# Performance work log

Hardware: AMD Instinct MI355X
Metric: run time of the kernel (lower is better)

Reference implementation:

```python
import jax, jax.numpy as jnp
import numpy as np

B, K, S, L, D, A = 16, 128, 64, 2, 256, 500  # batch, beam, stack, layers, hidden, max_actions


def setup_inputs() -> dict:
    key = jax.random.key(0)
    k = jax.random.split(key, 8)
    return {
        "gen_ll": jax.random.normal(k[0], (B, K), jnp.float32),
        "trees": jax.random.normal(k[1], (B, K, S, D), jnp.float32),
        "hiddens": jax.random.normal(k[2], (B, K, S + 1, L, D), jnp.float32),
        "cells": jax.random.normal(k[3], (B, K, S + 1, L, D), jnp.float32),
        "actions": jax.random.randint(k[4], (B, K, A), 0, 100, dtype=jnp.int64)
        if jax.config.jax_enable_x64 else jax.random.randint(k[4], (B, K, A), 0, 100),
        "actions_pos": jax.random.randint(k[5], (B, K), 0, A - 1),
        "pointer": jax.random.randint(k[6], (B, K), 0, S),
        "beam_widths": jax.random.randint(k[7], (B,), 1, K + 1),  # >= 1 active beam per batch
    }


def _gather_beam(x, sort_idx):
    # gather along beam dim (axis=1) with broadcast over trailing dims
    idx = sort_idx.reshape(sort_idx.shape + (1,) * (x.ndim - 2))
    return jnp.take_along_axis(x, idx, axis=1)


def reference(gen_ll, trees, hiddens, cells, actions, actions_pos, pointer, beam_widths):
    # BeamItems.shrink(): mask beams outside active width, sort by score desc,
    # then reorder every parallel tensor (stack + action path) by sort_idx.
    order = jnp.arange(K)
    active = order[None, :] < beam_widths[:, None]                    # [B, K] active_idx_mask
    gen_ll_m = jnp.where(active, gen_ll, -jnp.inf)
    sort_idx = jnp.argsort(-gen_ll_m, axis=1)                          # descending sort
    gen_ll_s = jnp.take_along_axis(gen_ll_m, sort_idx, axis=1)

    trees_s = _gather_beam(trees, sort_idx)                            # stack.sort_by
    hiddens_s = _gather_beam(hiddens, sort_idx)
    cells_s = _gather_beam(cells, sort_idx)
    actions_s = _gather_beam(actions, sort_idx)                        # action_path.sort_by
    actions_pos_s = jnp.take_along_axis(actions_pos, sort_idx, axis=1)
    pointer_s = jnp.take_along_axis(pointer, sort_idx, axis=1)         # stack_state.sort_by

    new_beam_widths = jnp.minimum(beam_widths, K)
    # BeamItems.marginal_probs(): logsumexp over active beams (inactive already -inf)
    marginal = jax.nn.logsumexp(gen_ll_s, axis=1)                      # [B]
    # ActionPath.prev_actions(): gather at actions_pos
    prev_actions = jnp.take_along_axis(actions_s, actions_pos_s[:, :, None], axis=2)[:, :, 0]

    return (gen_ll_s, trees_s, hiddens_s, cells_s, marginal,
            actions_s, actions_pos_s, pointer_s, prev_actions, new_beam_widths)
```

## Files before the change

kernel.cpp:

```cpp
#include <hip/hip_runtime.h>
#include <math.h>

#define B 16
#define K 128
#define S 64
#define L 2
#define D 256
#define A 500

#define ROW4_TREES 4096
#define ROW4_HID   8320
#define HALF4_HID  4160

#define NEG_BIG (-1.0e30f)

typedef float f32x4 __attribute__((ext_vector_type(4)));
typedef int   i32x4 __attribute__((ext_vector_type(4)));

#define OFF_GENLL 0
#define OFF_TREES 2048
#define OFF_HID   33556480
#define OFF_CELLS 101713920
#define OFF_MARG  169871360
#define OFF_ACT   169871376
#define OFF_APOS  170895376
#define OFF_PTR   170897424
#define OFF_PREV  170899472
#define OFF_NBW   170901520

#define NU_TREES 2048
#define NU_HC    8192
#define NU_BIG   (NU_TREES + NU_HC)
#define NB_ACT   (B * K)
#define GRID     (NU_BIG + NB_ACT + B)

template<int N4>
__device__ __forceinline__ void copy_unit(const f32x4* __restrict__ s,
                                          f32x4* __restrict__ d, int tid)
{
    constexpr int FULL = N4 / 256;
    constexpr int REM  = N4 % 256;
    for (int g = 0; g < FULL; g += 8) {
        f32x4 v[8];
#pragma unroll
        for (int i = 0; i < 8; ++i)
            v[i] = __builtin_nontemporal_load(&s[(g + i) * 256 + tid]);
#pragma unroll
        for (int i = 0; i < 8; ++i)
            __builtin_nontemporal_store(v[i], &d[(g + i) * 256 + tid]);
    }
    if (REM && tid < REM) {
        f32x4 v = __builtin_nontemporal_load(&s[FULL * 256 + tid]);
        __builtin_nontemporal_store(v, &d[FULL * 256 + tid]);
    }
}

__global__ void __launch_bounds__(256, 8)
k_fused(const float* __restrict__ gen_ll,
        const f32x4* __restrict__ trees,
        const f32x4* __restrict__ hiddens,
        const f32x4* __restrict__ cells,
        const int* __restrict__ actions,
        const int* __restrict__ actions_pos,
        const int* __restrict__ pointer,
        const int* __restrict__ beam_widths,
        float* __restrict__ out)
{
    __shared__ float key[K];
    __shared__ int   sidx[K];
    __shared__ float red[4];

    const int tid = threadIdx.x;
    const int bid = blockIdx.x;

    int type, b = 0, k = 0, r = 0;
    int which = 0, u2 = 0;
    if (bid < NU_BIG) {
        type = 2;
        if (bid < NU_TREES) {
            which = -1;
            r = bid; b = r >> 7; k = r & 127;
        } else {
            const int u = bid - NU_TREES;
            which = u >> 12;
            u2 = u & 4095;
            const int row = u2 >> 1;
            b = row >> 7; k = row & 127;
        }
    } else if (bid < NU_BIG + NB_ACT) {
        type = 1; r = bid - NU_BIG; b = r >> 7; k = r & 127;
    } else {
        type = 0; b = bid - (NU_BIG + NB_ACT);
    }

    const int w = beam_widths[b];
    if (tid < K) key[tid] = (tid < w) ? gen_ll[b * K + tid] : NEG_BIG;
    __syncthreads();
    if (tid < K) {
        const float my = key[tid];
        int rank = 0;
#pragma unroll 16
        for (int i = 0; i < K; ++i) {
            const float ki = key[i];
            rank += (ki > my) || (ki == my && i < tid);
        }
        sidx[rank] = tid;
    }
    __syncthreads();

    if (type == 2) {
        const int j = sidx[k];
        if (which < 0) {
            copy_unit<ROW4_TREES>(trees + (size_t)(b * K + j) * ROW4_TREES,
                                  (f32x4*)(out + OFF_TREES) + (size_t)r * ROW4_TREES,
                                  tid);
        } else {
            const int half = u2 & 1;
            const f32x4* src = (which ? cells : hiddens)
                             + ((size_t)(b * K + j) * 2 + half) * HALF4_HID;
            f32x4* dst = (f32x4*)(out + (which ? OFF_CELLS : OFF_HID))
                       + (size_t)u2 * HALF4_HID;
            copy_unit<HALF4_HID>(src, dst, tid);
        }
    } else if (type == 1) {
        const int j = sidx[k];
        const i32x4* s = (const i32x4*)actions + (size_t)(b * K + j) * 125;
        f32x4* d = (f32x4*)(out + OFF_ACT) + (size_t)r * 125;
        if (tid < 125) {
            const i32x4 v = __builtin_nontemporal_load(&s[tid]);
            f32x4 f;
            f.x = (float)v.x; f.y = (float)v.y; f.z = (float)v.z; f.w = (float)v.w;
            __builtin_nontemporal_store(f, &d[tid]);
        }
    } else {
        if (tid < K) {
            const int j = sidx[tid];
            out[OFF_GENLL + b * K + tid] = key[j];
            const int ap = actions_pos[b * K + j];
            out[OFF_APOS + b * K + tid] = (float)ap;
            out[OFF_PTR  + b * K + tid] = (float)pointer[b * K + j];
            out[OFF_PREV + b * K + tid] = (float)actions[(size_t)(b * K + j) * A + ap];
        }
        const float v = (tid < K) ? key[tid] : NEG_BIG;
        if (tid < 128) {
            float m = v;
#pragma unroll
            for (int mask = 32; mask >= 1; mask >>= 1)
                m = fmaxf(m, __shfl_xor(m, mask, 64));
            if ((tid & 63) == 0) red[tid >> 6] = m;
        }
        __syncthreads();
        const float m = fmaxf(red[0], red[1]);
        if (tid < 128) {
            float e = expf(v - m);
#pragma unroll
            for (int mask = 32; mask >= 1; mask >>= 1)
                e += __shfl_xor(e, mask, 64);
            if ((tid & 63) == 0) red[2 + (tid >> 6)] = e;
        }
        __syncthreads();
        if (tid == 0) {
            out[OFF_MARG + b] = m + logf(red[2] + red[3]);
            out[OFF_NBW + b] = (float)(w < K ? w : K);
        }
    }
}

extern "C" void kernel_launch(void* const* d_in, const int* in_sizes, int n_in,
                              void* d_out, int out_size, void* d_ws, size_t ws_size,
                              hipStream_t stream)
{
    const float* gen_ll      = (const float*)d_in[0];
    const float* trees       = (const float*)d_in[1];
    const float* hiddens     = (const float*)d_in[2];
    const float* cells       = (const float*)d_in[3];
    const int*   actions     = (const int*)d_in[4];
    const int*   actions_pos = (const int*)d_in[5];
    const int*   pointer     = (const int*)d_in[6];
    const int*   beam_widths = (const int*)d_in[7];
    float* out = (float*)d_out;

    k_fused<<<GRID, 256, 0, stream>>>(gen_ll, (const f32x4*)trees,
                                      (const f32x4*)hiddens, (const f32x4*)cells,
                                      actions, actions_pos, pointer, beam_widths, out);
}
```

Before: 259.8 us.

## Use fixed 2048-block grid with multiple copy units per block

Replaces one-block-per-unit launch (about 12k blocks) with 2048 persistent-style blocks that each copy five row units plus one actions row. Every block now ranks all 16 batches' keys in shared memory instead of one batch. The aim is to cut block launch and per-block sort overhead and amortize it over more copy work. In exchange, each block does sixteen times more redundant rank computation before it starts copying, and there is less block-level parallelism available to hide memory latency.

```diff
diff --git a/kernel.cpp b/kernel.cpp
--- a/kernel.cpp
+++ b/kernel.cpp
@@ -9,7 +9,6 @@
 #define A 500
 
 #define ROW4_TREES 4096
-#define ROW4_HID   8320
 #define HALF4_HID  4160
 
 #define NEG_BIG (-1.0e30f)
@@ -28,11 +27,9 @@
 #define OFF_PREV  170899472
 #define OFF_NBW   170901520
 
+#define NBLK 2048
 #define NU_TREES 2048
-#define NU_HC    8192
-#define NU_BIG   (NU_TREES + NU_HC)
-#define NB_ACT   (B * K)
-#define GRID     (NU_BIG + NB_ACT + B)
+#define UPB 5
 
 template<int N4>
 __device__ __forceinline__ void copy_unit(const f32x4* __restrict__ s,
@@ -66,82 +63,83 @@
         const int* __restrict__ beam_widths,
         float* __restrict__ out)
 {
-    __shared__ float key[K];
-    __shared__ int   sidx[K];
+    __shared__ float key[B][K];
+    __shared__ int   sidx[B][K];
+    __shared__ int   wbuf[B];
     __shared__ float red[4];
 
     const int tid = threadIdx.x;
     const int bid = blockIdx.x;
 
-    int type, b = 0, k = 0, r = 0;
-    int which = 0, u2 = 0;
-    if (bid < NU_BIG) {
-        type = 2;
-        if (bid < NU_TREES) {
-            which = -1;
-            r = bid; b = r >> 7; k = r & 127;
-        } else {
-            const int u = bid - NU_TREES;
-            which = u >> 12;
-            u2 = u & 4095;
-            const int row = u2 >> 1;
-            b = row >> 7; k = row & 127;
-        }
-    } else if (bid < NU_BIG + NB_ACT) {
-        type = 1; r = bid - NU_BIG; b = r >> 7; k = r & 127;
-    } else {
-        type = 0; b = bid - (NU_BIG + NB_ACT);
+    if (tid < B) wbuf[tid] = beam_widths[tid];
+    __syncthreads();
+    for (int t = tid; t < B * K; t += 256) {
+        const int b = t >> 7, i = t & 127;
+        key[b][i] = (i < wbuf[b]) ? gen_ll[t] : NEG_BIG;
     }
-
-    const int w = beam_widths[b];
-    if (tid < K) key[tid] = (tid < w) ? gen_ll[b * K + tid] : NEG_BIG;
     __syncthreads();
-    if (tid < K) {
-        const float my = key[tid];
+    for (int t = tid; t < B * K; t += 256) {
+        const int b = t >> 7, i = t & 127;
+        const float my = key[b][i];
         int rank = 0;
 #pragma unroll 16
-        for (int i = 0; i < K; ++i) {
-            const float ki = key[i];
-            rank += (ki > my) || (ki == my && i < tid);
+        for (int ii = 0; ii < K; ++ii) {
+            const float ki = key[b][ii];
+            rank += (ki > my) || (ki == my && ii < i);
         }
-        sidx[rank] = tid;
+        sidx[b][rank] = i;
     }
     __syncthreads();
 
-    if (type == 2) {
-        const int j = sidx[k];
-        if (which < 0) {
+    const int u0 = bid * UPB;
+#pragma unroll
+    for (int q = 0; q < UPB; ++q) {
+        const int u = u0 + q;
+        if (u < NU_TREES) {
+            const int b = u >> 7, k = u & 127;
+            const int j = sidx[b][k];
             copy_unit<ROW4_TREES>(trees + (size_t)(b * K + j) * ROW4_TREES,
-                                  (f32x4*)(out + OFF_TREES) + (size_t)r * ROW4_TREES,
+                                  (f32x4*)(out + OFF_TREES) + (size_t)u * ROW4_TREES,
                                   tid);
         } else {
-            const int half = u2 & 1;
+            const int u2 = u - NU_TREES;
+            const int which = u2 >> 12;
+            const int u3 = u2 & 4095;
+            const int row = u3 >> 1, half = u3 & 1;
+            const int b = row >> 7, k = row & 127;
+            const int j = sidx[b][k];
             const f32x4* src = (which ? cells : hiddens)
                              + ((size_t)(b * K + j) * 2 + half) * HALF4_HID;
             f32x4* dst = (f32x4*)(out + (which ? OFF_CELLS : OFF_HID))
-                       + (size_t)u2 * HALF4_HID;
+                       + (size_t)u3 * HALF4_HID;
             copy_unit<HALF4_HID>(src, dst, tid);
         }
-    } else if (type == 1) {
-        const int j = sidx[k];
+    }
+
+    {
+        const int b = bid >> 7, k = bid & 127;
+        const int j = sidx[b][k];
         const i32x4* s = (const i32x4*)actions + (size_t)(b * K + j) * 125;
-        f32x4* d = (f32x4*)(out + OFF_ACT) + (size_t)r * 125;
+        f32x4* d = (f32x4*)(out + OFF_ACT) + (size_t)bid * 125;
         if (tid < 125) {
             const i32x4 v = __builtin_nontemporal_load(&s[tid]);
             f32x4 f;
             f.x = (float)v.x; f.y = (float)v.y; f.z = (float)v.z; f.w = (float)v.w;
             __builtin_nontemporal_store(f, &d[tid]);
         }
-    } else {
+    }
+
+    if (bid < B) {
+        const int b = bid;
         if (tid < K) {
-            const int j = sidx[tid];
-            out[OFF_GENLL + b * K + tid] = key[j];
+            const int j = sidx[b][tid];
+            out[OFF_GENLL + b * K + tid] = key[b][j];
             const int ap = actions_pos[b * K + j];
             out[OFF_APOS + b * K + tid] = (float)ap;
             out[OFF_PTR  + b * K + tid] = (float)pointer[b * K + j];
             out[OFF_PREV + b * K + tid] = (float)actions[(size_t)(b * K + j) * A + ap];
         }
-        const float v = (tid < K) ? key[tid] : NEG_BIG;
+        const float v = (tid < K) ? key[b][tid] : NEG_BIG;
         if (tid < 128) {
             float m = v;
 #pragma unroll
@@ -161,6 +159,7 @@
         __syncthreads();
         if (tid == 0) {
             out[OFF_MARG + b] = m + logf(red[2] + red[3]);
+            const int w = wbuf[b];
             out[OFF_NBW + b] = (float)(w < K ? w : K);
         }
     }
@@ -180,7 +179,7 @@
     const int*   beam_widths = (const int*)d_in[7];
     float* out = (float*)d_out;
 
-    k_fused<<<GRID, 256, 0, stream>>>(gen_ll, (const f32x4*)trees,
+    k_fused<<<NBLK, 256, 0, stream>>>(gen_ll, (const f32x4*)trees,
                                       (const f32x4*)hiddens, (const f32x4*)cells,
                                       actions, actions_pos, pointer, beam_widths, out);
 }
```

Measured after the change: 288.2 us. +10.9%, slower.
